# Kernel tuning notes

Measured on AMD Instinct MI355X. Metric: run time of the kernel, lower is better.

## Reference

```python
import jax, jax.numpy as jnp
import numpy as np

B, NUM_ANCHORS, NUM_CLASSES = 32, 15130, 81
SCALE_XY, SCALE_WH = 0.1, 0.2
CRITERIA, MAX_OUT, SCORE_THRESH = 0.5, 200, 0.05


def setup_inputs() -> dict:
    key = jax.random.key(0)
    k1, k2, k3, k4 = jax.random.split(key, 4)
    ploc = jax.random.normal(k1, (B, 4, NUM_ANCHORS), dtype=jnp.float32)
    plabel = jax.random.normal(k2, (B, NUM_CLASSES, NUM_ANCHORS), dtype=jnp.float32)
    # default boxes in (cx, cy, w, h) form, all in [0, 1]
    xy = jax.random.uniform(k3, (NUM_ANCHORS, 2), dtype=jnp.float32, minval=0.05, maxval=0.95)
    wh = jax.random.uniform(k4, (NUM_ANCHORS, 2), dtype=jnp.float32, minval=0.02, maxval=0.3)
    dboxes_xywh = jnp.concatenate([xy, wh], axis=-1)
    return {"ploc": ploc, "plabel": plabel, "dboxes_xywh": dboxes_xywh}


def _iou(a, b):
    # a: [M,4] ltrb, b: [K,4] ltrb -> [M,K]
    lt = jnp.maximum(a[:, None, :2], b[None, :, :2])
    rb = jnp.minimum(a[:, None, 2:], b[None, :, 2:])
    wh = jnp.clip(rb - lt, 0.0)
    inter = wh[..., 0] * wh[..., 1]
    area_a = (a[:, 2] - a[:, 0]) * (a[:, 3] - a[:, 1])
    area_b = (b[:, 2] - b[:, 0]) * (b[:, 3] - b[:, 1])
    return inter / (area_a[:, None] + area_b[None, :] - inter + 1e-12)


def _decode(ploc, plabel, dboxes_xywh):
    # scale_back_batch: ploc [B,4,N] -> ltrb boxes [B,N,4]
    b = jnp.transpose(ploc, (0, 2, 1))
    xy = b[..., :2] * SCALE_XY * dboxes_xywh[:, 2:] + dboxes_xywh[:, :2]
    wh = jnp.exp(b[..., 2:] * SCALE_WH) * dboxes_xywh[:, 2:]
    ltrb = jnp.concatenate([xy - 0.5 * wh, xy + 0.5 * wh], axis=-1)  # [B,N,4]
    probs = jnp.transpose(jax.nn.softmax(plabel, axis=1), (0, 2, 1))  # [B,N,C]
    return ltrb, probs


def _nms_per_class(scores_c, boxes):
    # scores_c: [N], boxes: [N,4]
    s = jnp.where(scores_c > SCORE_THRESH, scores_c, 0.0)
    vals, idx = jax.lax.top_k(s, MAX_OUT)  # descending, matches score-sorted greedy order
    bx = boxes[idx]  # [MAX_OUT,4]
    iou = _iou(bx, bx)  # [MAX_OUT,MAX_OUT]
    later = jnp.arange(MAX_OUT)

    def body(i, keep):
        active = keep[i] & (vals[i] > 0.0)
        suppress = active & (iou[i] >= CRITERIA) & (later > i)
        return keep & ~suppress

    keep = jax.lax.fori_loop(0, MAX_OUT, body, jnp.ones((MAX_OUT,), bool))
    keep = keep & (vals > 0.0)
    return jnp.where(keep, vals, 0.0), bx


def _decode_single(probs_i, boxes_i):
    # skip background class 0
    cls_scores = probs_i[:, 1:].T  # [C-1, N]
    vals, bx = jax.vmap(_nms_per_class, in_axes=(0, None))(cls_scores, boxes_i)
    c1 = NUM_CLASSES - 1
    flat_v = vals.reshape(-1)                 # [(C-1)*MAX_OUT]
    flat_b = bx.reshape(-1, 4)
    labels = jnp.repeat(jnp.arange(1, c1 + 1, dtype=jnp.int32), MAX_OUT)
    top_v, top_i = jax.lax.top_k(flat_v, MAX_OUT)
    return flat_b[top_i], labels[top_i], top_v


def reference(ploc, plabel, dboxes_xywh):
    ltrb, probs = _decode(ploc, plabel, dboxes_xywh)
    boxes_out, labels_out, scores_out = jax.vmap(_decode_single)(probs, ltrb)
    return boxes_out, labels_out, scores_out
```

## Files before the change

kernel.cpp:

```cpp
#include <hip/hip_runtime.h>
#include <math.h>

namespace {
constexpr int BATCH = 32;
constexpr int NANCH = 15130;
constexpr int NCLS  = 81;
constexpr int C1    = 80;
constexpr int MAXO  = 200;
constexpr int APB   = 256;
constexpr int NBLKA = (NANCH + APB - 1) / APB;
constexpr int CAPK2 = 512;
constexpr int CAP   = 1024;
constexpr int CAPB  = 768;
constexpr int NBIN  = 2048;
constexpr int NBINK2 = 768;
constexpr unsigned BINBASE = 0x3D000000u;
constexpr int IMGCAP = C1 * MAXO;
}

#define SCORE_TH 0.05f
#define IOU_TH   0.5f

typedef unsigned long long u64;

__device__ __forceinline__ u64 shflx64(u64 v, int mask) {
    int lo = __shfl_xor((int)(unsigned)(v & 0xffffffffull), mask, 64);
    int hi = __shfl_xor((int)(unsigned)(v >> 32), mask, 64);
    return ((u64)(unsigned)hi << 32) | (unsigned)lo;
}

__device__ __forceinline__ void bitonic_desc(u64* keys, int P,
                                             int tid, int nthr) {
    for (int k = 2; k <= P; k <<= 1) {
        for (int j = k >> 1; j > 0; j >>= 1) {
            for (int i = tid; i < P; i += nthr) {
                int ixj = i ^ j;
                if (ixj > i) {
                    u64 a = keys[i], c = keys[ixj];
                    bool up = ((i & k) == 0);
                    if (up ? (a < c) : (a > c)) { keys[i] = c; keys[ixj] = a; }
                }
            }
            __syncthreads();
        }
    }
}

__device__ __forceinline__ u64 regsort256(u64 key, u64* lds, int tid) {
    for (int k = 2; k <= 256; k <<= 1) {
        for (int j = k >> 1; j > 0; j >>= 1) {
            u64 pv;
            if (j < 64) {
                pv = shflx64(key, j);
            } else {
                lds[tid] = key;
                __syncthreads();
                pv = lds[tid ^ j];
            }
            bool up = ((tid & k) == 0);
            bool lt = ((tid & j) == 0);
            u64 mx = (key > pv) ? key : pv;
            u64 mn = (key > pv) ? pv : key;
            key = (up == lt) ? mx : mn;
            if (j >= 64) __syncthreads();
        }
    }
    return key;
}

__device__ __forceinline__ bool iou_sup(const float4 bb, const float aa,
                                        const float4 bi, const float ai) {
#pragma clang fp contract(off)
    float l = fmaxf(bi.x, bb.x);
    float t = fmaxf(bi.y, bb.y);
    float r = fminf(bi.z, bb.z);
    float d = fminf(bi.w, bb.w);
    float in_ = fmaxf(r - l, 0.f) * fmaxf(d - t, 0.f);
    return (in_ / (ai + aa - in_ + 1e-12f)) >= IOU_TH;
}

__global__ __launch_bounds__(256, 3) void ssd_decode_stats(
    const float* __restrict__ ploc, const float* __restrict__ plabel,
    const float* __restrict__ dboxes,
    float* __restrict__ ltrb, float* __restrict__ rowmax,
    float* __restrict__ rowsum,
    int* __restrict__ cntg, u64* __restrict__ bucket) {
#pragma clang fp contract(off)
    __shared__ int lcnt[C1], lbase[C1], lrank[C1];

    const int tid = threadIdx.x;
    const int b   = blockIdx.x / NBLKA;
    const int n0  = (blockIdx.x % NBLKA) * APB;
    const int n   = n0 + tid;
    const bool act = (n < NANCH);

    if (tid < C1) lcnt[tid] = 0;

    float x[NCLS];
    if (act) {
        const float* pl = ploc + (size_t)b * 4 * NANCH + n;
        float px = pl[0], py = pl[NANCH], pw = pl[2 * NANCH],
              ph = pl[3 * NANCH];
        float4 db = reinterpret_cast<const float4*>(dboxes)[n];
        float cx = px * 0.1f * db.z + db.x;
        float cy = py * 0.1f * db.w + db.y;
        float w  = expf(pw * 0.2f) * db.z;
        float h  = expf(ph * 0.2f) * db.w;
        float4 o;
        o.x = cx - 0.5f * w; o.y = cy - 0.5f * h;
        o.z = cx + 0.5f * w; o.w = cy + 0.5f * h;
        reinterpret_cast<float4*>(ltrb)[(size_t)b * NANCH + n] = o;

        const float* pb = plabel + (size_t)b * NCLS * NANCH + n;
#pragma unroll
        for (int c = 0; c < NCLS; ++c) x[c] = pb[(size_t)c * NANCH];

        float m = -INFINITY;
#pragma unroll
        for (int c = 0; c < NCLS; ++c) m = fmaxf(m, x[c]);
#pragma unroll
        for (int c = 0; c < NCLS; ++c) x[c] = expf(x[c] - m);
        float s = 0.f;
#pragma unroll
        for (int c = 0; c < NCLS; ++c) s += x[c];
        rowmax[(size_t)b * NANCH + n] = m;
        rowsum[(size_t)b * NANCH + n] = s;

#pragma unroll
        for (int c = 1; c < NCLS; ++c) {
            x[c] = x[c] / s;
            if (x[c] > SCORE_TH) atomicAdd(&lcnt[c - 1], 1);
        }
    }
    __syncthreads();

    if (tid < C1) {
        int cn = lcnt[tid];
        lbase[tid] = (cn > 0) ? atomicAdd(&cntg[b * C1 + tid], cn) : 0;
        lrank[tid] = 0;
    }
    __syncthreads();

    if (act) {
#pragma unroll
        for (int c = 1; c < NCLS; ++c) {
            if (x[c] > SCORE_TH) {
                int r = atomicAdd(&lrank[c - 1], 1);
                int pos = lbase[c - 1] + r;
                if (pos < CAPB)
                    bucket[(size_t)(b * C1 + (c - 1)) * CAPB + pos] =
                        ((u64)__float_as_uint(x[c]) << 32)
                        | (u64)(0xFFFFFFFFu - (unsigned)n);
            }
        }
    }
}

__global__ __launch_bounds__(64) void ssd_class_nms(
    const float* __restrict__ plabel, const float* __restrict__ rowmax,
    const float* __restrict__ rowsum, const float* __restrict__ ltrb,
    const int* __restrict__ cntg, const u64* __restrict__ bucket,
    float* __restrict__ pcVals, float* __restrict__ pcBoxes,
    int* __restrict__ imgcnt, u64* __restrict__ imglist) {
    __shared__ u64 cand[CAPK2];
    __shared__ u64 pool[MAXO * 4];
    __shared__ float4 box4[MAXO];
    __shared__ float areas[MAXO];
    __shared__ int cnt, cutbin;

    unsigned* hist = (unsigned*)pool;

    const int lane = threadIdx.x;
    const int b    = blockIdx.x / C1;
    const int cls  = blockIdx.x % C1 + 1;
    const int bc   = b * C1 + (cls - 1);

    for (int i = lane; i < NBINK2; i += 64) hist[i] = 0u;
    if (lane == 0) { cnt = 0; cutbin = 1; }
    __syncthreads();

    const float* pl = plabel + ((size_t)b * NCLS + cls) * NANCH;
    const float* rm = rowmax + (size_t)b * NANCH;
    const float* rs = rowsum + (size_t)b * NANCH;
    const u64* bkt = bucket + (size_t)bc * CAPB;

    const int gcount = cntg[bc];
    const bool ovf = (gcount > CAPB);
    int gathered;

    if (!ovf) {
        for (int i = lane; i < gcount; i += 64) {
            unsigned bits = (unsigned)(bkt[i] >> 32);
            unsigned bin = ((bits - BINBASE) >> 16) + 1u;
            if (bin > NBINK2 - 1) bin = NBINK2 - 1;
            atomicAdd(&hist[bin], 1u);
        }
        __syncthreads();

        const int base = lane * 12;
        int loc = 0;
#pragma unroll
        for (int k = 0; k < 12; ++k) loc += (int)hist[base + k];
        int sfx = loc;
        for (int off = 1; off < 64; off <<= 1) {
            int t = __shfl_down(sfx, off, 64);
            if (lane + off < 64) sfx += t;
        }
        const int nztot = __shfl(sfx, 0);
        {
            int S = sfx - loc;
            for (int k = 11; k >= 0; --k) {
                int binv = (int)hist[base + k];
                int Sk = S + binv;
                int bin = base + k;
                if (bin >= 1 && Sk >= MAXO && S < MAXO) cutbin = bin;
                S = Sk;
            }
        }
        __syncthreads();
        const int B = (nztot >= MAXO) ? cutbin : 1;

        for (int i = lane; i < gcount; i += 64) {
            u64 k = bkt[i];
            unsigned bits = (unsigned)(k >> 32);
            unsigned bin = ((bits - BINBASE) >> 16) + 1u;
            if (bin > NBINK2 - 1) bin = NBINK2 - 1;
            if ((int)bin >= B) {
                int pos = atomicAdd(&cnt, 1);
                if (pos < CAPK2) cand[pos] = k;
            }
        }
        __syncthreads();
        gathered = min(cnt, CAPK2);
    } else {
        for (int n = lane; n < NANCH; n += 64) {
            float p = expf(pl[n] - rm[n]) / rs[n];
            if (p > SCORE_TH) {
                int pos = atomicAdd(&cnt, 1);
                if (pos < CAPK2)
                    cand[pos] = ((u64)__float_as_uint(p) << 32)
                              | (u64)(0xFFFFFFFFu - (unsigned)n);
            }
        }
        __syncthreads();
        gathered = min(cnt, CAPK2);
    }

    u64 r0, r1, r2, r3;
    if (gathered <= 256) {
        r0 = (lane < gathered) ? cand[lane] : 0ull;
        r1 = (64 + lane < gathered) ? cand[64 + lane] : 0ull;
        r2 = (128 + lane < gathered) ? cand[128 + lane] : 0ull;
        r3 = (192 + lane < gathered) ? cand[192 + lane] : 0ull;

        auto SH = [&](u64& rr, int j, bool up) {
            u64 pv = shflx64(rr, j);
            bool lt = ((lane & j) == 0);
            u64 mx = (rr > pv) ? rr : pv;
            u64 mn = (rr > pv) ? pv : rr;
            rr = (up == lt) ? mx : mn;
        };
        auto CE = [](u64& a, u64& c, bool up) {
            u64 mx = (a > c) ? a : c;
            u64 mn = (a > c) ? c : a;
            a = up ? mx : mn;
            c = up ? mn : mx;
        };
        for (int k = 2; k <= 32; k <<= 1) {
            for (int j = k >> 1; j > 0; j >>= 1) {
                bool up = ((lane & k) == 0);
                SH(r0, j, up); SH(r1, j, up); SH(r2, j, up); SH(r3, j, up);
            }
        }
        for (int j = 32; j > 0; j >>= 1) {
            SH(r0, j, true); SH(r1, j, false); SH(r2, j, true); SH(r3, j, false);
        }
        CE(r0, r1, true); CE(r2, r3, false);
        for (int j = 32; j > 0; j >>= 1) {
            SH(r0, j, true); SH(r1, j, true); SH(r2, j, false); SH(r3, j, false);
        }
        CE(r0, r2, true); CE(r1, r3, true);
        CE(r0, r1, true); CE(r2, r3, true);
        for (int j = 32; j > 0; j >>= 1) {
            SH(r0, j, true); SH(r1, j, true); SH(r2, j, true); SH(r3, j, true);
        }
    } else {
        for (int i = gathered + lane; i < CAPK2; i += 64) cand[i] = 0ull;
        __syncthreads();
        bitonic_desc(cand, CAPK2, lane, 64);
        r0 = cand[lane]; r1 = cand[64 + lane];
        r2 = cand[128 + lane]; r3 = cand[192 + lane];
    }

    if (gathered < MAXO) {
        cand[lane] = r0; cand[64 + lane] = r1;
        cand[128 + lane] = r2; cand[192 + lane] = r3;
        __syncthreads();
        const int need = MAXO - gathered;
        int fillcnt = 0;
        for (int base2 = 0; base2 < NANCH && fillcnt < need; base2 += 64) {
            int n = base2 + lane;
            bool flag = false;
            if (n < NANCH) {
                float p = expf(pl[n] - rm[n]) / rs[n];
                flag = (p <= SCORE_TH);
            }
            u64 bal = __ballot(flag);
            u64 below = (lane == 0) ? 0ull : (~0ull >> (64 - lane));
            int excl = (int)__popcll(bal & below);
            if (flag && (fillcnt + excl) < need)
                cand[gathered + fillcnt + excl] =
                    (u64)(0xFFFFFFFFu - (unsigned)n);
            fillcnt += (int)__popcll(bal);
        }
        __syncthreads();
        r0 = cand[lane]; r1 = cand[64 + lane];
        r2 = cand[128 + lane]; r3 = cand[192 + lane];
    }

    float4 b0, b1, b2, b3;
    float a0, a1, a2, a3, v0f, v1f, v2f, v3f;
    {
#pragma clang fp contract(off)
        const float4* lt4 = reinterpret_cast<const float4*>(ltrb)
                            + (size_t)b * NANCH;
        unsigned n0_ = 0xFFFFFFFFu - (unsigned)(r0 & 0xFFFFFFFFull);
        unsigned n1_ = 0xFFFFFFFFu - (unsigned)(r1 & 0xFFFFFFFFull);
        unsigned n2_ = 0xFFFFFFFFu - (unsigned)(r2 & 0xFFFFFFFFull);
        v0f = __uint_as_float((unsigned)(r0 >> 32));
        v1f = __uint_as_float((unsigned)(r1 >> 32));
        v2f = __uint_as_float((unsigned)(r2 >> 32));
        b0 = lt4[n0_]; b1 = lt4[n1_]; b2 = lt4[n2_];
        a0 = (b0.z - b0.x) * (b0.w - b0.y);
        a1 = (b1.z - b1.x) * (b1.w - b1.y);
        a2 = (b2.z - b2.x) * (b2.w - b2.y);
        box4[lane] = b0;        areas[lane] = a0;
        box4[64 + lane] = b1;   areas[64 + lane] = a1;
        box4[128 + lane] = b2;  areas[128 + lane] = a2;
        if (lane < MAXO - 192) {
            unsigned n3_ = 0xFFFFFFFFu - (unsigned)(r3 & 0xFFFFFFFFull);
            v3f = __uint_as_float((unsigned)(r3 >> 32));
            b3 = lt4[n3_];
            a3 = (b3.z - b3.x) * (b3.w - b3.y);
            box4[192 + lane] = b3;  areas[192 + lane] = a3;
        } else {
            v3f = 0.f; b3 = make_float4(0.f, 0.f, 0.f, 0.f); a3 = 0.f;
        }
    }
    const bool j3v = (lane < MAXO - 192);
    const u64 vm0 = __ballot(v0f > 0.f);
    const u64 vm1 = __ballot(v1f > 0.f);
    const u64 vm2 = __ballot(v2f > 0.f);
    const u64 vm3 = __ballot(j3v && (v3f > 0.f));
    __syncthreads();

    u64* supflat = pool;

    u64 nz0 = 0, nz1 = 0, nz2 = 0, nz3 = 0;
    for (int i = 0; i < 64; ++i) {
        float4 bi = box4[i]; float ai = areas[i];
        u64 s0 = __ballot(iou_sup(b0, a0, bi, ai) && (lane > i));
        u64 s1 = __ballot(iou_sup(b1, a1, bi, ai));
        u64 s2 = __ballot(iou_sup(b2, a2, bi, ai));
        u64 s3 = __ballot(iou_sup(b3, a3, bi, ai) && j3v);
        if ((s0 | s1 | s2 | s3) != 0ull) {
            nz0 |= 1ull << i;
            if (lane == 0) {
                supflat[i * 4 + 0] = s0; supflat[i * 4 + 1] = s1;
                supflat[i * 4 + 2] = s2; supflat[i * 4 + 3] = s3;
            }
        }
    }
    for (int i = 64; i < 128; ++i) {
        float4 bi = box4[i]; float ai = areas[i];
        u64 s1 = __ballot(iou_sup(b1, a1, bi, ai) && (64 + lane > i));
        u64 s2 = __ballot(iou_sup(b2, a2, bi, ai));
        u64 s3 = __ballot(iou_sup(b3, a3, bi, ai) && j3v);
        if ((s1 | s2 | s3) != 0ull) {
            nz1 |= 1ull << (i - 64);
            if (lane == 0) {
                supflat[i * 4 + 1] = s1;
                supflat[i * 4 + 2] = s2; supflat[i * 4 + 3] = s3;
            }
        }
    }
    for (int i = 128; i < 192; ++i) {
        float4 bi = box4[i]; float ai = areas[i];
        u64 s2 = __ballot(iou_sup(b2, a2, bi, ai) && (128 + lane > i));
        u64 s3 = __ballot(iou_sup(b3, a3, bi, ai) && j3v);
        if ((s2 | s3) != 0ull) {
            nz2 |= 1ull << (i - 128);
            if (lane == 0) {
                supflat[i * 4 + 2] = s2; supflat[i * 4 + 3] = s3;
            }
        }
    }
    for (int i = 192; i < MAXO; ++i) {
        float4 bi = box4[i]; float ai = areas[i];
        u64 s3 = __ballot(iou_sup(b3, a3, bi, ai) && j3v && (192 + lane > i));
        if (s3 != 0ull) {
            nz3 |= 1ull << (i - 192);
            if (lane == 0) supflat[i * 4 + 3] = s3;
        }
    }
    __syncthreads();

    u64 k0 = ~0ull, k1 = ~0ull, k2 = ~0ull, k3 = ~0ull;
    {
        int i = -1;
        u64 c;
        if ((c = k0 & vm0 & nz0))      i = __builtin_ctzll(c);
        else if ((c = k1 & vm1 & nz1)) i = 64 + __builtin_ctzll(c);
        else if ((c = k2 & vm2 & nz2)) i = 128 + __builtin_ctzll(c);
        else if ((c = k3 & vm3 & nz3)) i = 192 + __builtin_ctzll(c);
        while (i >= 0) {
            int wr = i >> 6, bit = i & 63;
            if (wr == 0) {
                k0 &= ~supflat[i * 4 + 0]; k1 &= ~supflat[i * 4 + 1];
                k2 &= ~supflat[i * 4 + 2]; k3 &= ~supflat[i * 4 + 3];
            } else if (wr == 1) {
                k1 &= ~supflat[i * 4 + 1];
                k2 &= ~supflat[i * 4 + 2]; k3 &= ~supflat[i * 4 + 3];
            } else if (wr == 2) {
                k2 &= ~supflat[i * 4 + 2]; k3 &= ~supflat[i * 4 + 3];
            } else {
                k3 &= ~supflat[i * 4 + 3];
            }
            u64 above = (bit == 63) ? 0ull : (~0ull << (bit + 1));
            u64 cur = ((wr == 0) ? (k0 & vm0 & nz0)
                     : (wr == 1) ? (k1 & vm1 & nz1)
                     : (wr == 2) ? (k2 & vm2 & nz2)
                                 : (k3 & vm3 & nz3)) & above;
            i = -1;
            while (true) {
                if (cur) { i = wr * 64 + __builtin_ctzll(cur); break; }
                if (++wr >= 4) break;
                cur = (wr == 1) ? (k1 & vm1 & nz1)
                    : (wr == 2) ? (k2 & vm2 & nz2) : (k3 & vm3 & nz3);
            }
        }
    }

    {
        float* pv  = pcVals + (size_t)bc * MAXO;
        float4* pb4 = reinterpret_cast<float4*>(pcBoxes + (size_t)bc * MAXO * 4);
        bool kp0 = (k0 >> lane) & 1ull, kp1 = (k1 >> lane) & 1ull;
        bool kp2 = (k2 >> lane) & 1ull, kp3 = (k3 >> lane) & 1ull;
        pv[lane]        = (kp0 && v0f > 0.f) ? v0f : 0.f;
        pv[64 + lane]   = (kp1 && v1f > 0.f) ? v1f : 0.f;
        pv[128 + lane]  = (kp2 && v2f > 0.f) ? v2f : 0.f;
        pb4[lane] = b0; pb4[64 + lane] = b1; pb4[128 + lane] = b2;
        if (j3v) {
            pv[192 + lane] = (kp3 && v3f > 0.f) ? v3f : 0.f;
            pb4[192 + lane] = b3;
        }
    }

    {
        u64 km0 = k0 & vm0, km1 = k1 & vm1, km2 = k2 & vm2, km3 = k3 & vm3;
        int c0 = (int)__popcll(km0), c1 = (int)__popcll(km1);
        int c2 = (int)__popcll(km2), c3 = (int)__popcll(km3);
        int tot = c0 + c1 + c2 + c3;
        int kb = 0;
        if (lane == 0 && tot > 0) kb = atomicAdd(&imgcnt[b], tot);
        kb = __shfl(kb, 0);
        u64 below = (lane == 0) ? 0ull : (~0ull >> (64 - lane));
        u64* dst = imglist + (size_t)b * IMGCAP + kb;
        const u64 himask = 0xFFFFFFFF00000000ull;
        if ((km0 >> lane) & 1ull) {
            unsigned g = (unsigned)((cls - 1) * MAXO + lane);
            dst[__popcll(km0 & below)] =
                (r0 & himask) | (u64)(0xFFFFFFFFu - g);
        }
        if ((km1 >> lane) & 1ull) {
            unsigned g = (unsigned)((cls - 1) * MAXO + 64 + lane);
            dst[c0 + __popcll(km1 & below)] =
                (r1 & himask) | (u64)(0xFFFFFFFFu - g);
        }
        if ((km2 >> lane) & 1ull) {
            unsigned g = (unsigned)((cls - 1) * MAXO + 128 + lane);
            dst[c0 + c1 + __popcll(km2 & below)] =
                (r2 & himask) | (u64)(0xFFFFFFFFu - g);
        }
        if ((km3 >> lane) & 1ull) {
            unsigned g = (unsigned)((cls - 1) * MAXO + 192 + lane);
            dst[c0 + c1 + c2 + __popcll(km3 & below)] =
                (r3 & himask) | (u64)(0xFFFFFFFFu - g);
        }
    }
}

__global__ __launch_bounds__(256) void ssd_final_topk(
    const float* __restrict__ pcVals, const float* __restrict__ pcBoxes,
    const int* __restrict__ imgcnt, const u64* __restrict__ imglist,
    float* __restrict__ out) {
    __shared__ unsigned int hist[NBIN];
    __shared__ u64 cand[CAP];
    __shared__ int wtot[4];
    __shared__ int cnt, cutbin, nztot;

    const int tid  = threadIdx.x;
    const int lane = tid & 63;
    const int wv   = tid >> 6;
    const int b    = blockIdx.x;
    const int TOT  = C1 * MAXO;
    const float* pv = pcVals + (size_t)b * TOT;
    const int NZ   = imgcnt[b];

    for (int i = tid; i < NBIN; i += 256) hist[i] = 0u;
    if (tid == 0) { cnt = 0; cutbin = 1; }
    __syncthreads();

    int count;
    if (NZ >= MAXO) {
        const u64* lst = imglist + (size_t)b * IMGCAP;
        for (int i = tid; i < NZ; i += 256) {
            unsigned bits = (unsigned)(lst[i] >> 32);
            unsigned bin = ((bits - BINBASE) >> 15) + 1u;
            if (bin > NBIN - 1) bin = NBIN - 1;
            atomicAdd(&hist[bin], 1u);
        }
        __syncthreads();

        const int base = tid * 8;
        int loc = 0;
        for (int k = 0; k < 8; ++k) loc += (int)hist[base + k];
        int sfx = loc;
        for (int off = 1; off < 64; off <<= 1) {
            int t = __shfl_down(sfx, off, 64);
            if (lane + off < 64) sfx += t;
        }
        if (lane == 0) wtot[wv] = sfx;
        __syncthreads();
        int crossSuf = 0;
        for (int w2 = wv + 1; w2 < 4; ++w2) crossSuf += wtot[w2];
        {
            int S = (sfx - loc) + crossSuf;
            for (int k = 7; k >= 0; --k) {
                int binv = (int)hist[base + k];
                int Sk = S + binv;
                int bin = base + k;
                if (bin >= 1 && Sk >= MAXO && S < MAXO) cutbin = bin;
                S = Sk;
            }
        }
        __syncthreads();
        const int B = cutbin;

        for (int i = tid; i < NZ; i += 256) {
            u64 k = lst[i];
            unsigned bits = (unsigned)(k >> 32);
            unsigned bin = ((bits - BINBASE) >> 15) + 1u;
            if (bin > NBIN - 1) bin = NBIN - 1;
            if ((int)bin >= B) {
                int pos = atomicAdd(&cnt, 1);
                if (pos < CAP) cand[pos] = k;
            }
        }
        __syncthreads();
        count = min(cnt, CAP);
    } else {
        for (int g = tid; g < TOT; g += 256) {
            float v = pv[g];
            if (v > 0.f) {
                unsigned bits = __float_as_uint(v);
                unsigned bin = ((bits - BINBASE) >> 15) + 1u;
                if (bin > NBIN - 1) bin = NBIN - 1;
                atomicAdd(&hist[bin], 1u);
            }
        }
        __syncthreads();
        const int base = tid * 8;
        int loc = 0;
        for (int k = 0; k < 8; ++k) loc += (int)hist[base + k];
        int sfx = loc;
        for (int off = 1; off < 64; off <<= 1) {
            int t = __shfl_down(sfx, off, 64);
            if (lane + off < 64) sfx += t;
        }
        if (lane == 0) wtot[wv] = sfx;
        __syncthreads();
        int crossSuf = 0;
        for (int w2 = wv + 1; w2 < 4; ++w2) crossSuf += wtot[w2];
        if (tid == 0) nztot = wtot[0] + wtot[1] + wtot[2] + wtot[3];
        {
            int S = (sfx - loc) + crossSuf;
            for (int k = 7; k >= 0; --k) {
                int binv = (int)hist[base + k];
                int Sk = S + binv;
                int bin = base + k;
                if (bin >= 1 && Sk >= MAXO && S < MAXO) cutbin = bin;
                S = Sk;
            }
        }
        __syncthreads();
        int B = (nztot >= MAXO) ? cutbin : 1;

        for (int g = tid; g < TOT; g += 256) {
            float v = pv[g];
            if (v > 0.f) {
                unsigned bits = __float_as_uint(v);
                unsigned bin = ((bits - BINBASE) >> 15) + 1u;
                if (bin > NBIN - 1) bin = NBIN - 1;
                if ((int)bin >= B) {
                    int pos = atomicAdd(&cnt, 1);
                    if (pos < CAP)
                        cand[pos] = ((u64)bits << 32)
                                  | (u64)(0xFFFFFFFFu - (unsigned)g);
                }
            }
        }
        __syncthreads();
        count = min(cnt, CAP);

        if (count < MAXO) {
            if (tid == 0) {
                int c = count;
                for (int g = 0; g < TOT && c < MAXO; ++g) {
                    if (!(pv[g] > 0.f)) {
                        cand[c++] = (u64)(0xFFFFFFFFu - (unsigned)g);
                    }
                }
                cnt = c;
            }
            __syncthreads();
            count = min(cnt, CAP);
        }
    }

    u64 key;
    if (count <= 256) {
        key = (tid < count) ? cand[tid] : 0ull;
        key = regsort256(key, cand, tid);
    } else {
        int P = 256; while (P < count) P <<= 1;
        for (int i = count + tid; i < P; i += 256) cand[i] = 0ull;
        __syncthreads();
        bitonic_desc(cand, P, tid, 256);
        key = cand[tid];
    }

    if (tid < MAXO) {
        float sc      = __uint_as_float((unsigned)(key >> 32));
        unsigned flat = 0xFFFFFFFFu - (unsigned)(key & 0xFFFFFFFFull);
        int cls = (int)(flat / MAXO) + 1;
        const float4 bb =
            reinterpret_cast<const float4*>(pcBoxes)[(size_t)b * TOT + flat];
        reinterpret_cast<float4*>(out)[(size_t)b * MAXO + tid] = bb;
        out[(size_t)BATCH * MAXO * 4 + (size_t)b * MAXO + tid] = (float)cls;
        out[(size_t)BATCH * MAXO * 5 + (size_t)b * MAXO + tid] = sc;
    }
}

extern "C" void kernel_launch(void* const* d_in, const int* in_sizes, int n_in,
                              void* d_out, int out_size, void* d_ws,
                              size_t ws_size, hipStream_t stream) {
    const float* ploc   = (const float*)d_in[0];
    const float* plabel = (const float*)d_in[1];
    const float* dboxes = (const float*)d_in[2];
    float* out = (float*)d_out;

    float* ws      = (float*)d_ws;
    float* ltrb    = ws;
    float* rowmax  = ltrb   + (size_t)BATCH * NANCH * 4;
    float* rowsum  = rowmax + (size_t)BATCH * NANCH;
    float* pcVals  = rowsum + (size_t)BATCH * NANCH;
    float* pcBoxes = pcVals + (size_t)BATCH * C1 * MAXO;
    int*   cntg    = (int*)(pcBoxes + (size_t)BATCH * C1 * MAXO * 4);
    int*   imgcnt  = cntg + BATCH * C1;
    char*  after   = (char*)(imgcnt + BATCH);
    u64* bucket = (u64*)(after + ((16 - (((size_t)after) & 15)) & 15));
    u64* imglist = bucket + (size_t)BATCH * C1 * CAPB;

    hipMemsetAsync(cntg, 0, (size_t)(BATCH * C1 + BATCH) * sizeof(int), stream);
    ssd_decode_stats<<<BATCH * NBLKA, APB, 0, stream>>>(
        ploc, plabel, dboxes, ltrb, rowmax, rowsum, cntg, bucket);
    ssd_class_nms<<<BATCH * C1, 64, 0, stream>>>(
        plabel, rowmax, rowsum, ltrb, cntg, bucket, pcVals, pcBoxes,
        imgcnt, imglist);
    ssd_final_topk<<<BATCH, 256, 0, stream>>>(
        pcVals, pcBoxes, imgcnt, imglist, out);
}
```

Measured before the change: 223.8 us.

## Replace divisions with multiply-compare plus exact fallback in softmax threshold and IoU tests

```diff
diff --git a/kernel.cpp b/kernel.cpp
--- a/kernel.cpp
+++ b/kernel.cpp
@@ -68,15 +68,16 @@
     return key;
 }
 
-__device__ __forceinline__ bool iou_sup(const float4 bb, const float aa,
-                                        const float4 bi, const float ai) {
+__device__ __forceinline__ void iou_parts(const float4 bb, const float aa,
+                                          const float4 bi, const float ai,
+                                          float& in_, float& dn) {
 #pragma clang fp contract(off)
     float l = fmaxf(bi.x, bb.x);
     float t = fmaxf(bi.y, bb.y);
     float r = fminf(bi.z, bb.z);
     float d = fminf(bi.w, bb.w);
-    float in_ = fmaxf(r - l, 0.f) * fmaxf(d - t, 0.f);
-    return (in_ / (ai + aa - in_ + 1e-12f)) >= IOU_TH;
+    in_ = fmaxf(r - l, 0.f) * fmaxf(d - t, 0.f);
+    dn  = ai + aa - in_ + 1e-12f;
 }
 
 __global__ __launch_bounds__(256, 3) void ssd_decode_stats(
@@ -97,6 +98,8 @@
     if (tid < C1) lcnt[tid] = 0;
 
     float x[NCLS];
+    float s = 1.f;
+    u64 w0 = 0, w1 = 0;
     if (act) {
         const float* pl = ploc + (size_t)b * 4 * NANCH + n;
         float px = pl[0], py = pl[NANCH], pw = pl[2 * NANCH],
@@ -120,16 +123,26 @@
         for (int c = 0; c < NCLS; ++c) m = fmaxf(m, x[c]);
 #pragma unroll
         for (int c = 0; c < NCLS; ++c) x[c] = expf(x[c] - m);
-        float s = 0.f;
+        s = 0.f;
 #pragma unroll
         for (int c = 0; c < NCLS; ++c) s += x[c];
         rowmax[(size_t)b * NANCH + n] = m;
         rowsum[(size_t)b * NANCH + n] = s;
 
+        const float sc = s * SCORE_TH;
+        const float lo = sc * 0.99999952f;
+        const float hi = sc * 1.00000048f;
 #pragma unroll
         for (int c = 1; c < NCLS; ++c) {
-            x[c] = x[c] / s;
-            if (x[c] > SCORE_TH) atomicAdd(&lcnt[c - 1], 1);
+            float e = x[c];
+            bool band = (e >= lo) && (e <= hi);
+            bool pass = (e > hi);
+            if (__any(band)) pass = band ? ((e / s) > SCORE_TH) : pass;
+            if (pass) {
+                atomicAdd(&lcnt[c - 1], 1);
+                if (c <= 64) w0 |= 1ull << (c - 1);
+                else         w1 |= 1ull << (c - 65);
+            }
         }
     }
     __syncthreads();
@@ -144,13 +157,17 @@
     if (act) {
 #pragma unroll
         for (int c = 1; c < NCLS; ++c) {
-            if (x[c] > SCORE_TH) {
+            bool pass = (c <= 64) ? ((w0 >> (c - 1)) & 1ull)
+                                  : ((w1 >> (c - 65)) & 1ull);
+            if (pass) {
                 int r = atomicAdd(&lrank[c - 1], 1);
                 int pos = lbase[c - 1] + r;
-                if (pos < CAPB)
+                if (pos < CAPB) {
+                    float p = x[c] / s;
                     bucket[(size_t)(b * C1 + (c - 1)) * CAPB + pos] =
-                        ((u64)__float_as_uint(x[c]) << 32)
+                        ((u64)__float_as_uint(p) << 32)
                         | (u64)(0xFFFFFFFFu - (unsigned)n);
+                }
             }
         }
     }
@@ -162,13 +179,14 @@
     const int* __restrict__ cntg, const u64* __restrict__ bucket,
     float* __restrict__ pcVals, float* __restrict__ pcBoxes,
     int* __restrict__ imgcnt, u64* __restrict__ imglist) {
-    __shared__ u64 cand[CAPK2];
     __shared__ u64 pool[MAXO * 4];
-    __shared__ float4 box4[MAXO];
-    __shared__ float areas[MAXO];
+    __shared__ __align__(16) u64 candbox[CAPK2];
     __shared__ int cnt, cutbin;
 
     unsigned* hist = (unsigned*)pool;
+    u64* cand = candbox;
+    float4* box4 = reinterpret_cast<float4*>(candbox);
+    float* areas = reinterpret_cast<float*>(candbox) + 800;
 
     const int lane = threadIdx.x;
     const int b    = blockIdx.x / C1;
@@ -334,17 +352,20 @@
         a0 = (b0.z - b0.x) * (b0.w - b0.y);
         a1 = (b1.z - b1.x) * (b1.w - b1.y);
         a2 = (b2.z - b2.x) * (b2.w - b2.y);
-        box4[lane] = b0;        areas[lane] = a0;
-        box4[64 + lane] = b1;   areas[64 + lane] = a1;
-        box4[128 + lane] = b2;  areas[128 + lane] = a2;
         if (lane < MAXO - 192) {
             unsigned n3_ = 0xFFFFFFFFu - (unsigned)(r3 & 0xFFFFFFFFull);
             v3f = __uint_as_float((unsigned)(r3 >> 32));
             b3 = lt4[n3_];
             a3 = (b3.z - b3.x) * (b3.w - b3.y);
-            box4[192 + lane] = b3;  areas[192 + lane] = a3;
         } else {
             v3f = 0.f; b3 = make_float4(0.f, 0.f, 0.f, 0.f); a3 = 0.f;
+        }
+        __syncthreads();
+        box4[lane] = b0;        areas[lane] = a0;
+        box4[64 + lane] = b1;   areas[64 + lane] = a1;
+        box4[128 + lane] = b2;  areas[128 + lane] = a2;
+        if (lane < MAXO - 192) {
+            box4[192 + lane] = b3;  areas[192 + lane] = a3;
         }
     }
     const bool j3v = (lane < MAXO - 192);
@@ -358,11 +379,29 @@
 
     u64 nz0 = 0, nz1 = 0, nz2 = 0, nz3 = 0;
     for (int i = 0; i < 64; ++i) {
+#pragma clang fp contract(off)
         float4 bi = box4[i]; float ai = areas[i];
-        u64 s0 = __ballot(iou_sup(b0, a0, bi, ai) && (lane > i));
-        u64 s1 = __ballot(iou_sup(b1, a1, bi, ai));
-        u64 s2 = __ballot(iou_sup(b2, a2, bi, ai));
-        u64 s3 = __ballot(iou_sup(b3, a3, bi, ai) && j3v);
+        float i0, d0_, i1, d1_, i2, d2_, i3, d3_;
+        iou_parts(b0, a0, bi, ai, i0, d0_);
+        iou_parts(b1, a1, bi, ai, i1, d1_);
+        iou_parts(b2, a2, bi, ai, i2, d2_);
+        iou_parts(b3, a3, bi, ai, i3, d3_);
+        float t0 = i0 + i0, t1 = i1 + i1, t2 = i2 + i2, t3 = i3 + i3;
+        bool su0 = t0 >= d0_, su1 = t1 >= d1_, su2 = t2 >= d2_, su3 = t3 >= d3_;
+        bool bd0 = !su0 && (t0 > d0_ * 0.99999952f);
+        bool bd1 = !su1 && (t1 > d1_ * 0.99999952f);
+        bool bd2 = !su2 && (t2 > d2_ * 0.99999952f);
+        bool bd3 = !su3 && (t3 > d3_ * 0.99999952f);
+        if (__any(bd0 | bd1 | bd2 | bd3)) {
+            su0 = bd0 ? (i0 / d0_ >= IOU_TH) : su0;
+            su1 = bd1 ? (i1 / d1_ >= IOU_TH) : su1;
+            su2 = bd2 ? (i2 / d2_ >= IOU_TH) : su2;
+            su3 = bd3 ? (i3 / d3_ >= IOU_TH) : su3;
+        }
+        u64 s0 = __ballot(su0 && (lane > i));
+        u64 s1 = __ballot(su1);
+        u64 s2 = __ballot(su2);
+        u64 s3 = __ballot(su3 && j3v);
         if ((s0 | s1 | s2 | s3) != 0ull) {
             nz0 |= 1ull << i;
             if (lane == 0) {
@@ -372,10 +411,25 @@
         }
     }
     for (int i = 64; i < 128; ++i) {
+#pragma clang fp contract(off)
         float4 bi = box4[i]; float ai = areas[i];
-        u64 s1 = __ballot(iou_sup(b1, a1, bi, ai) && (64 + lane > i));
-        u64 s2 = __ballot(iou_sup(b2, a2, bi, ai));
-        u64 s3 = __ballot(iou_sup(b3, a3, bi, ai) && j3v);
+        float i1, d1_, i2, d2_, i3, d3_;
+        iou_parts(b1, a1, bi, ai, i1, d1_);
+        iou_parts(b2, a2, bi, ai, i2, d2_);
+        iou_parts(b3, a3, bi, ai, i3, d3_);
+        float t1 = i1 + i1, t2 = i2 + i2, t3 = i3 + i3;
+        bool su1 = t1 >= d1_, su2 = t2 >= d2_, su3 = t3 >= d3_;
+        bool bd1 = !su1 && (t1 > d1_ * 0.99999952f);
+        bool bd2 = !su2 && (t2 > d2_ * 0.99999952f);
+        bool bd3 = !su3 && (t3 > d3_ * 0.99999952f);
+        if (__any(bd1 | bd2 | bd3)) {
+            su1 = bd1 ? (i1 / d1_ >= IOU_TH) : su1;
+            su2 = bd2 ? (i2 / d2_ >= IOU_TH) : su2;
+            su3 = bd3 ? (i3 / d3_ >= IOU_TH) : su3;
+        }
+        u64 s1 = __ballot(su1 && (64 + lane > i));
+        u64 s2 = __ballot(su2);
+        u64 s3 = __ballot(su3 && j3v);
         if ((s1 | s2 | s3) != 0ull) {
             nz1 |= 1ull << (i - 64);
             if (lane == 0) {
@@ -385,9 +439,21 @@
         }
     }
     for (int i = 128; i < 192; ++i) {
+#pragma clang fp contract(off)
         float4 bi = box4[i]; float ai = areas[i];
-        u64 s2 = __ballot(iou_sup(b2, a2, bi, ai) && (128 + lane > i));
-        u64 s3 = __ballot(iou_sup(b3, a3, bi, ai) && j3v);
+        float i2, d2_, i3, d3_;
+        iou_parts(b2, a2, bi, ai, i2, d2_);
+        iou_parts(b3, a3, bi, ai, i3, d3_);
+        float t2 = i2 + i2, t3 = i3 + i3;
+        bool su2 = t2 >= d2_, su3 = t3 >= d3_;
+        bool bd2 = !su2 && (t2 > d2_ * 0.99999952f);
+        bool bd3 = !su3 && (t3 > d3_ * 0.99999952f);
+        if (__any(bd2 | bd3)) {
+            su2 = bd2 ? (i2 / d2_ >= IOU_TH) : su2;
+            su3 = bd3 ? (i3 / d3_ >= IOU_TH) : su3;
+        }
+        u64 s2 = __ballot(su2 && (128 + lane > i));
+        u64 s3 = __ballot(su3 && j3v);
         if ((s2 | s3) != 0ull) {
             nz2 |= 1ull << (i - 128);
             if (lane == 0) {
@@ -396,8 +462,15 @@
         }
     }
     for (int i = 192; i < MAXO; ++i) {
+#pragma clang fp contract(off)
         float4 bi = box4[i]; float ai = areas[i];
-        u64 s3 = __ballot(iou_sup(b3, a3, bi, ai) && j3v && (192 + lane > i));
+        float i3, d3_;
+        iou_parts(b3, a3, bi, ai, i3, d3_);
+        float t3 = i3 + i3;
+        bool su3 = t3 >= d3_;
+        bool bd3 = !su3 && (t3 > d3_ * 0.99999952f);
+        if (__any(bd3)) su3 = bd3 ? (i3 / d3_ >= IOU_TH) : su3;
+        u64 s3 = __ballot(su3 && j3v && (192 + lane > i));
         if (s3 != 0ull) {
             nz3 |= 1ull << (i - 192);
             if (lane == 0) supflat[i * 4 + 3] = s3;
```

After: 219.2 us. 1.02x faster.
